# Kernel optimization log

Hardware: AMD Instinct MI355X
Metric: run time of the kernel (lower is better)

Reference implementation:

```python
import jax, jax.numpy as jnp
import numpy as np

NUM_NODES = 500000
INPUT_DIM = 256
ATTN_DIM = 64
NUM_GRAPHS = 512


def setup_inputs() -> dict:
    key = jax.random.key(0)
    ks = jax.random.split(key, 6)
    x = jax.random.normal(ks[0], (NUM_NODES, INPUT_DIM), dtype=jnp.float32)
    batch = jnp.sort(jax.random.randint(ks[1], (NUM_NODES,), 0, NUM_GRAPHS, dtype=jnp.int32)).astype(jnp.int64)
    # Xavier-uniform style init for linear weights, normal(0, 0.1) for context
    lim1 = float(np.sqrt(6.0 / (INPUT_DIM + ATTN_DIM)))
    W_att = jax.random.uniform(ks[2], (ATTN_DIM, INPUT_DIM), minval=-lim1, maxval=lim1, dtype=jnp.float32)
    b_att = jnp.zeros((ATTN_DIM,), dtype=jnp.float32)
    ctx = 0.1 * jax.random.normal(ks[3], (ATTN_DIM,), dtype=jnp.float32)
    lim2 = float(np.sqrt(6.0 / (INPUT_DIM + INPUT_DIM)))
    W_out = jax.random.uniform(ks[4], (INPUT_DIM, INPUT_DIM), minval=-lim2, maxval=lim2, dtype=jnp.float32)
    b_out = jnp.zeros((INPUT_DIM,), dtype=jnp.float32)
    return {"x": x, "batch": batch, "W_att": W_att, "b_att": b_att, "ctx": ctx, "W_out": W_out, "b_out": b_out}


def reference(x, batch, W_att, b_att, ctx, W_out, b_out):
    seg = batch.astype(jnp.int32)
    # attention scores per node: tanh(x W^T + b) . ctx  -> [N]
    logits = jnp.tanh(x @ W_att.T + b_att)
    scores = logits @ ctx  # [N]
    # segment-wise stable softmax
    seg_max = jax.ops.segment_max(scores, seg, num_segments=NUM_GRAPHS)
    exp_s = jnp.exp(scores - seg_max[seg])
    seg_sum = jax.ops.segment_sum(exp_s, seg, num_segments=NUM_GRAPHS)
    w = exp_s / (seg_sum[seg] + 1e-8)  # [N]
    # weighted segment-sum pooling -> [B, D]
    pooled = jax.ops.segment_sum(x * w[:, None], seg, num_segments=NUM_GRAPHS)
    return pooled @ W_out.T + b_out
```

## Files before the change

kernel.cpp:

```cpp
#include <hip/hip_runtime.h>
#include <hip/hip_bf16.h>
#include <math.h>

#define N_NODES 500000
#define DIM 256
#define ADIM 64
#define NG 512
#define TILE 32
#define NTILES 15625
#define GRID_F 768

typedef __attribute__((ext_vector_type(8))) short short8;
typedef __attribute__((ext_vector_type(4))) float floatx4;

#define BAR() asm volatile("s_waitcnt lgkmcnt(0)\n\ts_barrier" ::: "memory")

__device__ inline unsigned short f2bf(float f) {
    union { float f; unsigned int u; } v; v.f = f;
    unsigned int u = v.u;
    unsigned int r = u + 0x7FFFu + ((u >> 16) & 1u);
    return (unsigned short)(r >> 16);
}

__device__ inline unsigned pk_bf2(float a, float b) {
    __hip_bfloat162 h = __float22bfloat162_rn(make_float2(a, b));
    union { __hip_bfloat162 h; unsigned u; } cv; cv.h = h;
    return cv.u;
}

__device__ inline float tanh_fast(float xv) {
    float e = __expf(2.0f * fabsf(xv));
    float r = 1.0f - 2.0f * __builtin_amdgcn_rcpf(e + 1.0f);
    return copysignf(r, xv);
}

__global__ __launch_bounds__(256) void k_prep(const float* __restrict__ W_out,
                                              const float* __restrict__ W_att,
                                              const float* __restrict__ ctx,
                                              float* __restrict__ Wt_out,
                                              unsigned short* __restrict__ Wbf,
                                              float* __restrict__ cnorm,
                                              float* __restrict__ zero_base) {
    int b = blockIdx.x, t = threadIdx.x;
    if (b < 256) {
        int idx = b * 256 + t;
        int o = idx >> 8, d = idx & 255;
        Wt_out[d * DIM + o] = W_out[idx];
    } else if (b < 320) {
        int idx = (b - 256) * 256 + t;
        Wbf[idx] = f2bf(W_att[idx]);
    } else if (b < 834) {
        int idx = (b - 320) * 256 + t;
        zero_base[idx] = 0.f;
    } else if (t == 0) {
        float s = 0.f;
        for (int k = 0; k < ADIM; ++k) s += fabsf(ctx[k]);
        *cnorm = s;
    }
}

__global__ __launch_bounds__(256, 3) void k_fused(const float* __restrict__ x,
                                                  const unsigned short* __restrict__ Wbf,
                                                  const float* __restrict__ b_att,
                                                  const float* __restrict__ ctx,
                                                  const int* __restrict__ batch,
                                                  const float* __restrict__ cnorm,
                                                  float* __restrict__ accum,
                                                  float* __restrict__ ssum) {
    __shared__ __align__(16) unsigned short xs[2][8][33][40];
    __shared__ float sacc[4][32];
    __shared__ float pbuf[32];
    __shared__ int   gbuf[32];
    __shared__ __align__(16) float redp[4][DIM];

    const int t = threadIdx.x;
    const int wave = t >> 6;
    const int lane = t & 63;
    const int quad = lane >> 4;
    const int lcol = lane & 15;
    const float cn = *cnorm;

    const int b = blockIdx.x;
    const int q = NTILES / GRID_F, r = NTILES % GRID_F;
    const int t0 = b * q + min(b, r);
    const int t1 = t0 + q + (b < r ? 1 : 0);

    short8 bfrag[8];
    {
        const unsigned short* wr = Wbf + (size_t)(16 * wave + lcol) * DIM + quad * 8;
#pragma unroll
        for (int s = 0; s < 8; ++s) bfrag[s] = *(const short8*)(wr + s * 32);
    }

    const int srow = t >> 3;
    const int soff = (t & 7) * 4;
    const int ps = lane >> 3;
    const int pc = (lane & 7) * 4;

    const float ctxv = ctx[16 * wave + lcol];
    const float bv = b_att[16 * wave + lcol];

    float4 a4 = make_float4(0.f, 0.f, 0.f, 0.f);
    float s_acc = 0.f;
    int cur_g = -1;
    int cur = 0;

    auto FLUSH = [&](int gf) {
        *(float4*)&redp[wave][(lane >> 3) * 32 + (lane & 7) * 4] = a4;
        BAR();
        float rsum = (redp[0][t] + redp[1][t]) + (redp[2][t] + redp[3][t]);
        atomicAdd(&accum[(size_t)gf * DIM + t], rsum);
        if (t < 64) {
            float sp = (t < 32) ? s_acc : 0.f;
            sp += __shfl_xor(sp, 1);  sp += __shfl_xor(sp, 2);
            sp += __shfl_xor(sp, 4);  sp += __shfl_xor(sp, 8);
            sp += __shfl_xor(sp, 16);
            if (t == 0) atomicAdd(&ssum[gf], sp);
        }
        BAR();
    };

    {
        const float* xrow = x + (size_t)(t0 * TILE + srow) * DIM + soff;
        float4 h0[8];
#pragma unroll
        for (int s = 0; s < 8; ++s) h0[s] = *(const float4*)(xrow + s * 32);
#pragma unroll
        for (int s = 0; s < 8; ++s) {
            uint2 w;
            w.x = pk_bf2(h0[s].x, h0[s].y);
            w.y = pk_bf2(h0[s].z, h0[s].w);
            *(uint2*)&xs[0][s][srow][soff] = w;
        }
        BAR();
    }

    float4 h[8];
    for (int ti = t0; ti < t1; ++ti) {
        const bool haveNext = (ti + 1 < t1);
        if (haveNext) {
            const float* xrow = x + (size_t)((ti + 1) * TILE + srow) * DIM + soff;
#pragma unroll
            for (int s = 0; s < 8; ++s) h[s] = *(const float4*)(xrow + s * 32);
        }
        const int bval = batch[ti * TILE + (t & 31)];

        floatx4 acc[2];
        acc[0] = (floatx4)0.f; acc[1] = (floatx4)0.f;
#pragma unroll
        for (int s = 0; s < 8; ++s) {
#pragma unroll
            for (int mt = 0; mt < 2; ++mt) {
                short8 afrag = *(const short8*)&xs[cur][s][mt * 16 + lcol][quad * 8];
                acc[mt] = __builtin_amdgcn_mfma_f32_16x16x32_bf16(afrag, bfrag[s], acc[mt], 0, 0, 0);
            }
        }

#pragma unroll
        for (int mt = 0; mt < 2; ++mt) {
#pragma unroll
            for (int r4 = 0; r4 < 4; ++r4) {
                float v = ctxv * tanh_fast(acc[mt][r4] + bv);
                v += __shfl_xor(v, 1);
                v += __shfl_xor(v, 2);
                v += __shfl_xor(v, 4);
                v += __shfl_xor(v, 8);
                if (lcol == 0) sacc[wave][mt * 16 + quad * 4 + r4] = v;
            }
        }
        BAR();

        if (t < 32) {
            float sres = (sacc[0][t] + sacc[1][t]) + (sacc[2][t] + sacc[3][t]);
            pbuf[t] = __expf(sres - cn);
            gbuf[t] = bval;
        }
        if (haveNext) {
#pragma unroll
            for (int s = 0; s < 8; ++s) {
                uint2 w;
                w.x = pk_bf2(h[s].x, h[s].y);
                w.y = pk_bf2(h[s].z, h[s].w);
                *(uint2*)&xs[cur ^ 1][s][srow][soff] = w;
            }
        }
        BAR();

        const int g0 = gbuf[0];
        const int g1 = gbuf[31];
        if (cur_g < 0) cur_g = g0;
        for (int g = cur_g; g <= g1; ++g) {
#pragma unroll
            for (int j = 0; j < 8; ++j) {
                int i = (wave << 3) + j;
                float wp = (gbuf[i] == g) ? pbuf[i] : 0.f;
                if (wp != 0.f) {
                    uint2 v = *(const uint2*)&xs[cur][ps][i][pc];
                    a4.x += wp * __uint_as_float(v.x << 16);
                    a4.y += wp * __uint_as_float(v.x & 0xffff0000u);
                    a4.z += wp * __uint_as_float(v.y << 16);
                    a4.w += wp * __uint_as_float(v.y & 0xffff0000u);
                }
            }
            if (t < 32) s_acc += (gbuf[t] == g) ? pbuf[t] : 0.f;
            if (g < g1) {
                FLUSH(g);
                a4 = make_float4(0.f, 0.f, 0.f, 0.f);
                s_acc = 0.f;
            }
        }
        cur_g = g1;
        cur ^= 1;
    }
    FLUSH(cur_g);
}

__global__ __launch_bounds__(256) void k_out(const float* __restrict__ accum,
                                             const float* __restrict__ ssum,
                                             const float* __restrict__ WtOut,
                                             const float* __restrict__ b_out,
                                             float* __restrict__ out) {
    int g = blockIdx.x;
    int t = threadIdx.x;
    __shared__ float pl[256];
    float inv = 1.0f / (ssum[g] + 1e-20f);
    pl[t] = accum[(size_t)g * DIM + t] * inv;
    __syncthreads();
    float acc = b_out[t];
#pragma unroll 4
    for (int d = 0; d < DIM; ++d) acc += pl[d] * WtOut[d * DIM + t];
    out[(size_t)g * DIM + t] = acc;
}

extern "C" void kernel_launch(void* const* d_in, const int* in_sizes, int n_in,
                              void* d_out, int out_size, void* d_ws, size_t ws_size,
                              hipStream_t stream) {
    (void)in_sizes; (void)n_in; (void)out_size; (void)ws_size;
    const float* x     = (const float*)d_in[0];
    const int*   batch = (const int*)d_in[1];
    const float* W_att = (const float*)d_in[2];
    const float* b_att = (const float*)d_in[3];
    const float* ctx   = (const float*)d_in[4];
    const float* W_out = (const float*)d_in[5];
    const float* b_out = (const float*)d_in[6];
    float* out = (float*)d_out;

    float* accum = (float*)d_ws;
    float* ssum  = accum + 131072;
    float* Wt    = ssum + 512;
    unsigned short* Wbf = (unsigned short*)(Wt + 65536);
    float* cnorm = (float*)(Wbf + 16384);

    k_prep<<<dim3(835), dim3(256), 0, stream>>>(W_out, W_att, ctx, Wt, Wbf, cnorm, accum);
    k_fused<<<dim3(GRID_F), dim3(256), 0, stream>>>(x, Wbf, b_att, ctx, batch, cnorm, accum, ssum);
    k_out<<<dim3(NG), dim3(256), 0, stream>>>(accum, ssum, Wt, b_out, out);
}
```

Before: 707.5 us.

## Stage fp32 x tiles directly into LDS via async global_load_lds with swizzle

Replaces the register-staged bf16 conversion of x tiles with direct global-to-LDS async loads of fp32 rows, using an XOR swizzle to avoid bank conflicts. The bf16 packing now happens at fragment-load time before the MFMA, and pooling reads fp32 from LDS, which improves pooling precision. Grid shrinks to 512 blocks because the larger fp32 double buffer (about 70KB dynamic LDS) limits occupancy. Shuffle reductions become DPP row adds. The aim is to cut register pressure and VALU conversion work on the load path and overlap the next tile's load with compute, at the cost of lower occupancy and extra LDS traffic.

Measured after the change: 709.3 us. Within noise of the previous version (+0.3%).

```diff
diff --git a/kernel.cpp b/kernel.cpp
--- a/kernel.cpp
+++ b/kernel.cpp
@@ -8,12 +8,20 @@
 #define NG 512
 #define TILE 32
 #define NTILES 15625
-#define GRID_F 768
+#define GRID_F 512
+
+#define OFF_XSF   0
+#define OFF_REDP  65536
+#define OFF_SACC  69632
+#define OFF_PBUF  70144
+#define OFF_GBUF  70272
+#define SMEM_BYTES 70656
 
 typedef __attribute__((ext_vector_type(8))) short short8;
 typedef __attribute__((ext_vector_type(4))) float floatx4;
 
 #define BAR() asm volatile("s_waitcnt lgkmcnt(0)\n\ts_barrier" ::: "memory")
+#define VMWAIT0() asm volatile("s_waitcnt vmcnt(0)" ::: "memory")
 
 __device__ inline unsigned short f2bf(float f) {
     union { float f; unsigned int u; } v; v.f = f;
@@ -32,6 +40,21 @@
     float e = __expf(2.0f * fabsf(xv));
     float r = 1.0f - 2.0f * __builtin_amdgcn_rcpf(e + 1.0f);
     return copysignf(r, xv);
+}
+
+template <int CTRL>
+__device__ inline float dpp_add(float v) {
+    union { float f; int i; } a, b;
+    a.f = v;
+    b.i = __builtin_amdgcn_update_dpp(0, a.i, CTRL, 0xF, 0xF, true);
+    return v + b.f;
+}
+__device__ inline float row16_sum(float v) {
+    v = dpp_add<0xB1>(v);
+    v = dpp_add<0x4E>(v);
+    v = dpp_add<0x124>(v);
+    v = dpp_add<0x128>(v);
+    return v;
 }
 
 __global__ __launch_bounds__(256) void k_prep(const float* __restrict__ W_out,
@@ -59,25 +82,40 @@
     }
 }
 
-__global__ __launch_bounds__(256, 3) void k_fused(const float* __restrict__ x,
-                                                  const unsigned short* __restrict__ Wbf,
-                                                  const float* __restrict__ b_att,
-                                                  const float* __restrict__ ctx,
-                                                  const int* __restrict__ batch,
-                                                  const float* __restrict__ cnorm,
-                                                  float* __restrict__ accum,
-                                                  float* __restrict__ ssum) {
-    __shared__ __align__(16) unsigned short xs[2][8][33][40];
-    __shared__ float sacc[4][32];
-    __shared__ float pbuf[32];
-    __shared__ int   gbuf[32];
-    __shared__ __align__(16) float redp[4][DIM];
+__device__ inline void stage_tile(const float* __restrict__ x, float* xsf_buf,
+                                  int tile, int wave, int lane) {
+#pragma unroll
+    for (int r = 0; r < 8; ++r) {
+        const int row = wave * 8 + r;
+        const float* gsrc = x + (size_t)(tile * TILE + row) * DIM + ((lane ^ r) << 2);
+        __builtin_amdgcn_global_load_lds(
+            (const __attribute__((address_space(1))) unsigned int*)gsrc,
+            (__attribute__((address_space(3))) unsigned int*)(xsf_buf + row * DIM),
+            16, 0, 0);
+    }
+}
+
+__global__ __launch_bounds__(256) void k_fused(const float* __restrict__ x,
+                                               const unsigned short* __restrict__ Wbf,
+                                               const float* __restrict__ b_att,
+                                               const float* __restrict__ ctx,
+                                               const int* __restrict__ batch,
+                                               const float* __restrict__ cnorm,
+                                               float* __restrict__ accum,
+                                               float* __restrict__ ssum) {
+    extern __shared__ __align__(16) char smem[];
+    float* xsf  = (float*)(smem + OFF_XSF);
+    float* redp = (float*)(smem + OFF_REDP);
+    float* sacc = (float*)(smem + OFF_SACC);
+    float* pbuf = (float*)(smem + OFF_PBUF);
+    int*   gbuf = (int*)(smem + OFF_GBUF);
 
     const int t = threadIdx.x;
     const int wave = t >> 6;
     const int lane = t & 63;
     const int quad = lane >> 4;
     const int lcol = lane & 15;
+    const int m = lcol & 7;
     const float cn = *cnorm;
 
     const int b = blockIdx.x;
@@ -92,11 +130,6 @@
         for (int s = 0; s < 8; ++s) bfrag[s] = *(const short8*)(wr + s * 32);
     }
 
-    const int srow = t >> 3;
-    const int soff = (t & 7) * 4;
-    const int ps = lane >> 3;
-    const int pc = (lane & 7) * 4;
-
     const float ctxv = ctx[16 * wave + lcol];
     const float bv = b_att[16 * wave + lcol];
 
@@ -106,9 +139,9 @@
     int cur = 0;
 
     auto FLUSH = [&](int gf) {
-        *(float4*)&redp[wave][(lane >> 3) * 32 + (lane & 7) * 4] = a4;
-        BAR();
-        float rsum = (redp[0][t] + redp[1][t]) + (redp[2][t] + redp[3][t]);
+        *(float4*)(redp + wave * DIM + (lane << 2)) = a4;
+        BAR();
+        float rsum = (redp[t] + redp[DIM + t]) + (redp[2 * DIM + t] + redp[3 * DIM + t]);
         atomicAdd(&accum[(size_t)gf * DIM + t], rsum);
         if (t < 64) {
             float sp = (t < 32) ? s_acc : 0.f;
@@ -120,39 +153,31 @@
         BAR();
     };
 
-    {
-        const float* xrow = x + (size_t)(t0 * TILE + srow) * DIM + soff;
-        float4 h0[8];
-#pragma unroll
-        for (int s = 0; s < 8; ++s) h0[s] = *(const float4*)(xrow + s * 32);
-#pragma unroll
-        for (int s = 0; s < 8; ++s) {
-            uint2 w;
-            w.x = pk_bf2(h0[s].x, h0[s].y);
-            w.y = pk_bf2(h0[s].z, h0[s].w);
-            *(uint2*)&xs[0][s][srow][soff] = w;
-        }
-        BAR();
-    }
-
-    float4 h[8];
+    stage_tile(x, xsf, t0, wave, lane);
+    VMWAIT0();
+    BAR();
+
     for (int ti = t0; ti < t1; ++ti) {
         const bool haveNext = (ti + 1 < t1);
-        if (haveNext) {
-            const float* xrow = x + (size_t)((ti + 1) * TILE + srow) * DIM + soff;
-#pragma unroll
-            for (int s = 0; s < 8; ++s) h[s] = *(const float4*)(xrow + s * 32);
-        }
+        float* xcur = xsf + cur * (TILE * DIM);
+
+        if (haveNext) stage_tile(x, xsf + (cur ^ 1) * (TILE * DIM), ti + 1, wave, lane);
         const int bval = batch[ti * TILE + (t & 31)];
 
-        floatx4 acc[2];
-        acc[0] = (floatx4)0.f; acc[1] = (floatx4)0.f;
+        floatx4 acc0 = (floatx4)0.f, acc1 = (floatx4)0.f;
 #pragma unroll
         for (int s = 0; s < 8; ++s) {
+            const int q0 = s * 8 + quad * 2;
 #pragma unroll
             for (int mt = 0; mt < 2; ++mt) {
-                short8 afrag = *(const short8*)&xs[cur][s][mt * 16 + lcol][quad * 8];
-                acc[mt] = __builtin_amdgcn_mfma_f32_16x16x32_bf16(afrag, bfrag[s], acc[mt], 0, 0, 0);
+                const float* rowp = xcur + (mt * 16 + lcol) * DIM;
+                float4 f0 = *(const float4*)(rowp + (((q0    ) ^ m) << 2));
+                float4 f1 = *(const float4*)(rowp + (((q0 + 1) ^ m) << 2));
+                union { short8 v; unsigned u[4]; } au;
+                au.u[0] = pk_bf2(f0.x, f0.y); au.u[1] = pk_bf2(f0.z, f0.w);
+                au.u[2] = pk_bf2(f1.x, f1.y); au.u[3] = pk_bf2(f1.z, f1.w);
+                if (mt == 0) acc0 = __builtin_amdgcn_mfma_f32_16x16x32_bf16(au.v, bfrag[s], acc0, 0, 0, 0);
+                else         acc1 = __builtin_amdgcn_mfma_f32_16x16x32_bf16(au.v, bfrag[s], acc1, 0, 0, 0);
             }
         }
 
@@ -160,29 +185,17 @@
         for (int mt = 0; mt < 2; ++mt) {
 #pragma unroll
             for (int r4 = 0; r4 < 4; ++r4) {
-                float v = ctxv * tanh_fast(acc[mt][r4] + bv);
-                v += __shfl_xor(v, 1);
-                v += __shfl_xor(v, 2);
-                v += __shfl_xor(v, 4);
-                v += __shfl_xor(v, 8);
-                if (lcol == 0) sacc[wave][mt * 16 + quad * 4 + r4] = v;
+                float av = (mt == 0) ? acc0[r4] : acc1[r4];
+                float v = row16_sum(ctxv * tanh_fast(av + bv));
+                if (lcol == 0) sacc[wave * 32 + mt * 16 + quad * 4 + r4] = v;
             }
         }
         BAR();
 
         if (t < 32) {
-            float sres = (sacc[0][t] + sacc[1][t]) + (sacc[2][t] + sacc[3][t]);
+            float sres = (sacc[t] + sacc[32 + t]) + (sacc[64 + t] + sacc[96 + t]);
             pbuf[t] = __expf(sres - cn);
             gbuf[t] = bval;
-        }
-        if (haveNext) {
-#pragma unroll
-            for (int s = 0; s < 8; ++s) {
-                uint2 w;
-                w.x = pk_bf2(h[s].x, h[s].y);
-                w.y = pk_bf2(h[s].z, h[s].w);
-                *(uint2*)&xs[cur ^ 1][s][srow][soff] = w;
-            }
         }
         BAR();
 
@@ -192,14 +205,14 @@
         for (int g = cur_g; g <= g1; ++g) {
 #pragma unroll
             for (int j = 0; j < 8; ++j) {
-                int i = (wave << 3) + j;
-                float wp = (gbuf[i] == g) ? pbuf[i] : 0.f;
+                const int i = (wave << 3) + j;
+                const float wp = (gbuf[i] == g) ? pbuf[i] : 0.f;
                 if (wp != 0.f) {
-                    uint2 v = *(const uint2*)&xs[cur][ps][i][pc];
-                    a4.x += wp * __uint_as_float(v.x << 16);
-                    a4.y += wp * __uint_as_float(v.x & 0xffff0000u);
-                    a4.z += wp * __uint_as_float(v.y << 16);
-                    a4.w += wp * __uint_as_float(v.y & 0xffff0000u);
+                    const float4 v = *(const float4*)(xcur + i * DIM + ((lane ^ j) << 2));
+                    a4.x += wp * v.x;
+                    a4.y += wp * v.y;
+                    a4.z += wp * v.z;
+                    a4.w += wp * v.w;
                 }
             }
             if (t < 32) s_acc += (gbuf[t] == g) ? pbuf[t] : 0.f;
@@ -210,6 +223,9 @@
             }
         }
         cur_g = g1;
+
+        if (haveNext) VMWAIT0();
+        BAR();
         cur ^= 1;
     }
     FLUSH(cur_g);
@@ -251,7 +267,10 @@
     unsigned short* Wbf = (unsigned short*)(Wt + 65536);
     float* cnorm = (float*)(Wbf + 16384);
 
+    hipFuncSetAttribute((const void*)k_fused,
+                        hipFuncAttributeMaxDynamicSharedMemorySize, SMEM_BYTES);
+
     k_prep<<<dim3(835), dim3(256), 0, stream>>>(W_out, W_att, ctx, Wt, Wbf, cnorm, accum);
-    k_fused<<<dim3(GRID_F), dim3(256), 0, stream>>>(x, Wbf, b_att, ctx, batch, cnorm, accum, ssum);
+    k_fused<<<dim3(GRID_F), dim3(256), SMEM_BYTES, stream>>>(x, Wbf, b_att, ctx, batch, cnorm, accum, ssum);
     k_out<<<dim3(NG), dim3(256), 0, stream>>>(accum, ssum, Wt, b_out, out);
 }
```
